# Kernel optimization log

Measured on AMD Instinct MI355X. Metric: run time of the kernel, lower is better.

The kernel has to match this reference:

```python
import jax, jax.numpy as jnp
import numpy as np

B, N, C = 2, 8192, 256
H = 8
CH = C // H  # head dim 32
M = 32       # nbhd size
HID = 512    # mlp hidden = 2.0 * dim
TAB = 3025   # pre_table rows (55x55 relative positions)
POSF = 5     # pos_dim + 3


def _ln(x, w, b):
    mu = jnp.mean(x, axis=-1, keepdims=True)
    var = jnp.var(x, axis=-1, keepdims=True)
    return (x - mu) / jnp.sqrt(var + 1e-5) * w + b


def setup_inputs() -> dict:
    key = jax.random.key(0)
    ks = jax.random.split(key, 24)
    s = lambda fan: 1.0 / np.sqrt(fan)
    inp = {
        'feat': jax.random.normal(ks[0], (B, N, C), jnp.float32),
        'member_idx': jax.random.randint(ks[1], (B, N, M), 0, N),
        'cluster_mask': jnp.ones((B, N, M), jnp.float32),
        'pe_idx': jax.random.randint(ks[2], (B, N, M), 0, TAB),
        'global_attn': 0,
        'pre_table': jax.random.normal(ks[3], (TAB, POSF), jnp.float32),
        'norm1_w': jnp.ones((C,), jnp.float32),
        'norm1_b': jnp.zeros((C,), jnp.float32),
        'q_w': jax.random.normal(ks[4], (C, C), jnp.float32) * s(C),
        'q_b': jnp.zeros((C,), jnp.float32),
        'kv_w': jax.random.normal(ks[5], (2 * C, C), jnp.float32) * s(C),
        'kv_b': jnp.zeros((2 * C,), jnp.float32),
        'blank_k': jax.random.normal(ks[6], (C,), jnp.float32),
        'blank_v': jax.random.normal(ks[7], (C,), jnp.float32),
        'pe_w': jax.random.normal(ks[8], (H, POSF), jnp.float32) * s(POSF),
        'pe_b': jnp.zeros((H,), jnp.float32),
        'proj_w': jax.random.normal(ks[9], (C, C), jnp.float32) * s(C),
        'proj_b': jnp.zeros((C,), jnp.float32),
        'norm2_w': jnp.ones((C,), jnp.float32),
        'norm2_b': jnp.zeros((C,), jnp.float32),
        'fc1_w': jax.random.normal(ks[10], (HID, C), jnp.float32) * s(C),
        'fc1_b': jnp.zeros((HID,), jnp.float32),
        'fc2_w': jax.random.normal(ks[11], (C, HID), jnp.float32) * s(HID),
        'fc2_b': jnp.zeros((C,), jnp.float32),
    }
    return inp


def _block(feat, member_idx, cluster_mask, pe_idx, pre_table,
           norm1_w, norm1_b, q_w, q_b, kv_w, kv_b, blank_k, blank_v,
           pe_w, pe_b, proj_w, proj_b, norm2_w, norm2_b,
           fc1_w, fc1_b, fc2_w, fc2_b):
    b, n, c = feat.shape
    h, c_ = H, c // H
    scale = c_ ** -0.5
    shortcut = feat
    x = _ln(feat, norm1_w, norm1_b)
    q = (x @ q_w.T + q_b) * scale                     # b n c
    kv = (x @ kv_w.T + kv_b).reshape(b, n, h, 2, c_)  # torch view layout
    k = kv[..., 0, :]                                 # b n h c_
    v = kv[..., 1, :]
    q = q.reshape(b, n, h, c_)
    bidx = jnp.arange(b)[:, None, None]
    k_g = k[bidx, member_idx]                         # b n m h c_ (gather)
    attn = jnp.einsum('bnhc,bnmhc->bhnm', q, k_g)     # CLUSTENQK
    pe_table = pre_table @ pe_w.T + pe_b              # TAB h
    pos = pe_table[pe_idx]                            # b n m h
    attn = attn + pos.transpose(0, 3, 1, 2)
    attn = attn + (1.0 - cluster_mask)[:, None, :, :] * (-100.0)
    blank = jnp.einsum('bnhc,hc->bhn', q, blank_k.reshape(h, c_))
    blank = jnp.clip(blank, -5.0, 5.0)[..., None]     # b h n 1
    attn = jnp.concatenate([attn, blank], axis=-1)
    attn = jax.nn.softmax(attn, axis=-1)
    blank_a = attn[..., -1:]
    attn = attn[..., :-1]
    v_g = v[bidx, member_idx]                         # b n m h c_
    out = jnp.einsum('bhnm,bnmhc->bnhc', attn, v_g)   # CLUSTENAV
    out = out + blank_a.transpose(0, 2, 1, 3) * blank_v.reshape(1, 1, h, c_)
    out = out.reshape(b, n, c)
    out = out @ proj_w.T + proj_b
    x = shortcut + out
    y = _ln(x, norm2_w, norm2_b)
    y = jax.nn.gelu(y @ fc1_w.T + fc1_b, approximate=False)
    y = y @ fc2_w.T + fc2_b
    return x + y


def reference(feat, member_idx, cluster_mask, pe_idx, global_attn, pre_table,
              norm1_w, norm1_b, q_w, q_b, kv_w, kv_b, blank_k, blank_v,
              pe_w, pe_b, proj_w, proj_b, norm2_w, norm2_b,
              fc1_w, fc1_b, fc2_w, fc2_b):
    # global_attn is False (local cluster attention path)
    return _block(feat, member_idx, cluster_mask, pe_idx, pre_table,
                  norm1_w, norm1_b, q_w, q_b, kv_w, kv_b, blank_k, blank_v,
                  pe_w, pe_b, proj_w, proj_b, norm2_w, norm2_b,
                  fc1_w, fc1_b, fc2_w, fc2_b)
```

## Files before the change

kernel.cpp:

```cpp
#include <hip/hip_runtime.h>
#include <math.h>

namespace {
constexpr int kN    = 8192;
constexpr int kC    = 256;
constexpr int kTAB  = 3025;
constexpr int kRowsTotal = 2 * kN;
constexpr float kScale = 0.17677669529663687f;
}

typedef __attribute__((ext_vector_type(8))) short bf16x8;
typedef __attribute__((ext_vector_type(4))) float f32x4;

__device__ __forceinline__ unsigned short f2bf(float f) {
  unsigned int u = __float_as_uint(f);
  u += 0x7fffu + ((u >> 16) & 1u);
  return (unsigned short)(u >> 16);
}
__device__ __forceinline__ float bflo(unsigned int u) {
  return __uint_as_float(u << 16);
}
__device__ __forceinline__ float bfhi(unsigned int u) {
  return __uint_as_float(u & 0xffff0000u);
}

#define GLOAD16(g, l)                                                   \
  __builtin_amdgcn_global_load_lds(                                     \
      (const __attribute__((address_space(1))) void*)(g),               \
      (__attribute__((address_space(3))) void*)(l), 16, 0, 0)

__global__ __launch_bounds__(256) void ln_bf16_kernel(
    const float* __restrict__ x, const float* __restrict__ w,
    const float* __restrict__ b, unsigned short* __restrict__ o) {
  int t = threadIdx.x;
  int row = blockIdx.x * 4 + (t >> 6);
  int l = t & 63;
  float4 v = *(const float4*)(x + (size_t)row * kC + l * 4);
  float s  = v.x + v.y + v.z + v.w;
  float s2 = v.x * v.x + v.y * v.y + v.z * v.z + v.w * v.w;
#pragma unroll
  for (int d = 1; d < 64; d <<= 1) {
    s  += __shfl_xor(s, d, 64);
    s2 += __shfl_xor(s2, d, 64);
  }
  float mu = s * (1.0f / kC);
  float rstd = rsqrtf(s2 * (1.0f / kC) - mu * mu + 1e-5f);
  float4 wv = *(const float4*)(w + l * 4);
  float4 bv = *(const float4*)(b + l * 4);
  unsigned short o0 = f2bf((v.x - mu) * rstd * wv.x + bv.x);
  unsigned short o1 = f2bf((v.y - mu) * rstd * wv.y + bv.y);
  unsigned short o2 = f2bf((v.z - mu) * rstd * wv.z + bv.z);
  unsigned short o3 = f2bf((v.w - mu) * rstd * wv.w + bv.w);
  uint2 ov;
  ov.x = ((unsigned int)o1 << 16) | o0;
  ov.y = ((unsigned int)o3 << 16) | o2;
  *(uint2*)(o + (size_t)row * kC + l * 4) = ov;
}

__global__ __launch_bounds__(256) void pe_kernel(const float* __restrict__ tab,
                                                 const float* __restrict__ pw,
                                                 const float* __restrict__ pb,
                                                 float* __restrict__ outp) {
  int i = blockIdx.x * 256 + threadIdx.x;
  if (i >= kTAB * 8) return;
  int r = i >> 3, h = i & 7;
  float acc = pb[h];
#pragma unroll
  for (int f = 0; f < 5; ++f) acc += tab[r * 5 + f] * pw[h * 5 + f];
  outp[i] = acc;
}

__global__ __launch_bounds__(256) void cast_weights_kernel(
    const float* __restrict__ qw, const float* __restrict__ kvw,
    const float* __restrict__ pjw, const float* __restrict__ f1w,
    const float* __restrict__ f2w, const float* __restrict__ qb,
    const float* __restrict__ kvb, unsigned short* __restrict__ wqkv,
    unsigned short* __restrict__ wproj, unsigned short* __restrict__ wfc1,
    unsigned short* __restrict__ wfc2, float* __restrict__ bqkv) {
  int i = blockIdx.x * 256 + threadIdx.x;
  if (i < 65536)       wqkv[i]            = f2bf(qw[i]);
  else if (i < 196608) wqkv[i]            = f2bf(kvw[i - 65536]);
  else if (i < 262144) wproj[i - 196608]  = f2bf(pjw[i - 196608]);
  else if (i < 393216) wfc1[i - 262144]   = f2bf(f1w[i - 262144]);
  else if (i < 524288) wfc2[i - 393216]   = f2bf(f2w[i - 393216]);
  else if (i < 524544) bqkv[i - 524288]   = qb[i - 524288];
  else if (i < 525056) bqkv[i - 524288]   = kvb[i - 524544];
}

template <int EPI, int KDIM>
__global__ __launch_bounds__(512) void gemm64(
    const unsigned short* __restrict__ A, const unsigned short* __restrict__ Wt,
    const float* __restrict__ bias, void* __restrict__ o1,
    unsigned short* __restrict__ o2, unsigned short* __restrict__ o3,
    const float* __restrict__ res, const float* __restrict__ w2,
    const float* __restrict__ b2, unsigned short* __restrict__ yln) {
  __shared__ alignas(16) unsigned short smem[40960];
  unsigned short* As0 = smem;
  unsigned short* Bs0 = smem + 8192;
  int t = threadIdx.x;
  int w = t >> 6, l = t & 63;
  int bm = blockIdx.x * 64, bn = blockIdx.y * 256;

  f32x4 acc[4][2] = {};

  const size_t aoff = (size_t)(bm + w * 8 + (l >> 3)) * KDIM + (l & 7) * 8;
  const size_t boff = (size_t)(bn + w * 32 + (l >> 3)) * KDIM + (l & 7) * 8;
  const int lr = l & 15, lk = l >> 4;

#define STAGE_T(buf, k0)                                                      \
  do {                                                                        \
    GLOAD16(A + aoff + (k0), As0 + (buf)*4096 + w * 512 + l * 8);             \
    GLOAD16(Wt + boff + (k0), Bs0 + (buf)*16384 + w * 2048 + l * 8);          \
    GLOAD16(Wt + boff + (k0) + (size_t)8 * KDIM,                              \
            Bs0 + (buf)*16384 + w * 2048 + 512 + l * 8);                      \
    GLOAD16(Wt + boff + (k0) + (size_t)16 * KDIM,                             \
            Bs0 + (buf)*16384 + w * 2048 + 1024 + l * 8);                     \
    GLOAD16(Wt + boff + (k0) + (size_t)24 * KDIM,                             \
            Bs0 + (buf)*16384 + w * 2048 + 1536 + l * 8);                     \
  } while (0)

  auto compute = [&](int buf) {
#pragma unroll
    for (int kk = 0; kk < 2; ++kk) {
      bf16x8 af[4], bfr[2];
#pragma unroll
      for (int mi = 0; mi < 4; ++mi)
        af[mi] = *(const bf16x8*)(As0 + buf * 4096 + (mi * 16 + lr) * 64 +
                                  kk * 32 + lk * 8);
#pragma unroll
      for (int ni = 0; ni < 2; ++ni)
        bfr[ni] = *(const bf16x8*)(Bs0 + buf * 16384 +
                                   (w * 32 + ni * 16 + lr) * 64 + kk * 32 +
                                   lk * 8);
#pragma unroll
      for (int mi = 0; mi < 4; ++mi)
#pragma unroll
        for (int ni = 0; ni < 2; ++ni)
          acc[mi][ni] = __builtin_amdgcn_mfma_f32_16x16x32_bf16(
              af[mi], bfr[ni], acc[mi][ni], 0, 0, 0);
    }
  };

  STAGE_T(0, 0);
  __syncthreads();
  int cur = 0;
#pragma unroll
  for (int k0 = 64; k0 < KDIM; k0 += 64) {
    STAGE_T(cur ^ 1, k0);
    compute(cur);
    __syncthreads();
    cur ^= 1;
  }
  compute(cur);

  if constexpr (EPI == 1) {
    __syncthreads();
    float* xs = (float*)smem;
#pragma unroll
    for (int mi = 0; mi < 4; ++mi) {
#pragma unroll
      for (int ni = 0; ni < 2; ++ni) {
        int c = w * 32 + ni * 16 + lr;
        float bv = bias[c];
#pragma unroll
        for (int j = 0; j < 4; ++j) {
          int rl = mi * 16 + lk * 4 + j;
          float x = acc[mi][ni][j] + bv + res[(size_t)(bm + rl) * 256 + c];
          xs[rl * 260 + c] = x;
          ((float*)o1)[(size_t)(bm + rl) * 256 + c] = x;
        }
      }
    }
    __syncthreads();
    int r = t >> 3, sub = t & 7;
    float4 xv[8];
    float sx = 0.f, sxx = 0.f;
#pragma unroll
    for (int i = 0; i < 8; ++i) {
      xv[i] = *(const float4*)&xs[r * 260 + sub * 4 + i * 32];
      sx  += xv[i].x + xv[i].y + xv[i].z + xv[i].w;
      sxx += xv[i].x * xv[i].x + xv[i].y * xv[i].y + xv[i].z * xv[i].z +
             xv[i].w * xv[i].w;
    }
#pragma unroll
    for (int d = 1; d < 8; d <<= 1) {
      sx  += __shfl_xor(sx, d, 64);
      sxx += __shfl_xor(sxx, d, 64);
    }
    float mu = sx * (1.0f / 256.0f);
    float rstd = rsqrtf(sxx * (1.0f / 256.0f) - mu * mu + 1e-5f);
#pragma unroll
    for (int i = 0; i < 8; ++i) {
      int c = sub * 4 + i * 32;
      float4 wv = *(const float4*)(w2 + c);
      float4 bv = *(const float4*)(b2 + c);
      unsigned short y0 = f2bf((xv[i].x - mu) * rstd * wv.x + bv.x);
      unsigned short y1 = f2bf((xv[i].y - mu) * rstd * wv.y + bv.y);
      unsigned short y2 = f2bf((xv[i].z - mu) * rstd * wv.z + bv.z);
      unsigned short y3 = f2bf((xv[i].w - mu) * rstd * wv.w + bv.w);
      uint2 ov;
      ov.x = ((unsigned int)y1 << 16) | y0;
      ov.y = ((unsigned int)y3 << 16) | y2;
      *(uint2*)(yln + (size_t)(bm + r) * 256 + c) = ov;
    }
  } else {
#pragma unroll
    for (int mi = 0; mi < 4; ++mi) {
#pragma unroll
      for (int ni = 0; ni < 2; ++ni) {
        int col = bn + w * 32 + ni * 16 + lr;
        float bv = bias[col];
#pragma unroll
        for (int j = 0; j < 4; ++j) {
          int rg = bm + mi * 16 + lk * 4 + j;
          float x = acc[mi][ni][j] + bv;
          if constexpr (EPI == 0) {
            if (col < 256) {
              ((unsigned short*)o1)[(size_t)rg * 256 + col] = f2bf(x * kScale);
            } else {
              int c = col - 256;
              int h = c >> 6, sbit = (c >> 5) & 1, ch = c & 31;
              unsigned short* dst = sbit ? o3 : o2;
              dst[(size_t)rg * 256 + h * 32 + ch] = f2bf(x);
            }
          } else if constexpr (EPI == 2) {
            float g = 0.5f * x * (1.0f + erff(x * 0.70710678118654752f));
            ((unsigned short*)o1)[(size_t)rg * 512 + col] = f2bf(g);
          } else {
            ((float*)o1)[(size_t)rg * 256 + col] =
                res[(size_t)rg * 256 + col] + x;
          }
        }
      }
    }
  }
#undef STAGE_T
}

__global__ __launch_bounds__(256) void attn_kernel(
    const unsigned short* __restrict__ q, const unsigned short* __restrict__ k,
    const unsigned short* __restrict__ v, const int* __restrict__ member_idx,
    const int* __restrict__ pe_idx, const float* __restrict__ cmask,
    const float* __restrict__ pe_full, const float* __restrict__ blank_k,
    const float* __restrict__ blank_v, unsigned short* __restrict__ outp) {
  int t = threadIdx.x;
  int w = t >> 6, l = t & 63;
  int bid = blockIdx.x;
  int part = bid & 7;
  int bb = part >> 2, hg = part & 3;
  int row = bb * kN + (bid >> 3) * 4 + w;
  const unsigned int kvbyte = (unsigned int)bb * (kN * 512u);
  const int hloc = l >> 5, m = l & 31;
  const int head = hg * 2 + hloc;

  __shared__ float        qs[4][64];
  __shared__ float        aw[4][2][34];
  __shared__ unsigned int offs[4][32];

  qs[w][l] = bflo((unsigned int)q[(size_t)row * 256 + hg * 64 + l]);
  int   idxv = member_idx[(size_t)row * 32 + m];
  float mk   = (1.0f - cmask[(size_t)row * 32 + m]) * -100.0f;
  float pe   = pe_full[(size_t)pe_idx[(size_t)row * 32 + m] * 8 + head];
  if (l < 32) offs[w][l] = kvbyte + (unsigned int)idxv * 512u;
  __syncthreads();

  float4 qv[8];
#pragma unroll
  for (int i = 0; i < 8; ++i) qv[i] = *(const float4*)&qs[w][hloc * 32 + i * 4];

  unsigned int koff = kvbyte + (unsigned int)idxv * 512u;
  const char* kp = (const char*)k + koff + head * 64;
  float lg = 0.f;
#pragma unroll
  for (int j = 0; j < 4; ++j) {
    uint4 u = *(const uint4*)(kp + j * 16);
    lg = fmaf(qv[2 * j].x, bflo(u.x), lg);
    lg = fmaf(qv[2 * j].y, bfhi(u.x), lg);
    lg = fmaf(qv[2 * j].z, bflo(u.y), lg);
    lg = fmaf(qv[2 * j].w, bfhi(u.y), lg);
    lg = fmaf(qv[2 * j + 1].x, bflo(u.z), lg);
    lg = fmaf(qv[2 * j + 1].y, bfhi(u.z), lg);
    lg = fmaf(qv[2 * j + 1].z, bflo(u.w), lg);
    lg = fmaf(qv[2 * j + 1].w, bfhi(u.w), lg);
  }
  lg += mk + pe;

  float bl = qs[w][hloc * 32 + m] * blank_k[head * 32 + m];
#pragma unroll
  for (int d = 1; d < 32; d <<= 1) bl += __shfl_xor(bl, d, 64);
  bl = fminf(fmaxf(bl, -5.0f), 5.0f);

  float mx = lg;
#pragma unroll
  for (int d = 1; d < 32; d <<= 1) mx = fmaxf(mx, __shfl_xor(mx, d, 64));
  mx = fmaxf(mx, bl);
  float e = __expf(lg - mx);
  float s = e;
#pragma unroll
  for (int d = 1; d < 32; d <<= 1) s += __shfl_xor(s, d, 64);
  float eb = __expf(bl - mx);
  s += eb;
  float inv = __builtin_amdgcn_rcpf(s);
  aw[w][hloc][m] = e * inv;
  if (m == 0) aw[w][hloc][32] = eb * inv;
  __syncthreads();

  const int hp = l >> 5, sq = (l >> 3) & 3, c8 = l & 7;
  const char* vb = (const char*)v + (hg * 2 + hp) * 64 + c8 * 8;
  float a0 = 0.f, a1 = 0.f, a2 = 0.f, a3 = 0.f;
#pragma unroll
  for (int i = 0; i < 8; ++i) {
    int mm = sq * 8 + i;
    float a = aw[w][hp][mm];
    uint2 u = *(const uint2*)(vb + offs[w][mm]);
    a0 = fmaf(a, bflo(u.x), a0);
    a1 = fmaf(a, bfhi(u.x), a1);
    a2 = fmaf(a, bflo(u.y), a2);
    a3 = fmaf(a, bfhi(u.y), a3);
  }
  a0 += __shfl_xor(a0, 8, 64);  a1 += __shfl_xor(a1, 8, 64);
  a2 += __shfl_xor(a2, 8, 64);  a3 += __shfl_xor(a3, 8, 64);
  a0 += __shfl_xor(a0, 16, 64); a1 += __shfl_xor(a1, 16, 64);
  a2 += __shfl_xor(a2, 16, 64); a3 += __shfl_xor(a3, 16, 64);
  if (sq == 0) {
    float ab = aw[w][hp][32];
    int c = (hg * 2 + hp) * 32 + c8 * 4;
    float4 bv = *(const float4*)(blank_v + c);
    a0 = fmaf(ab, bv.x, a0);
    a1 = fmaf(ab, bv.y, a1);
    a2 = fmaf(ab, bv.z, a2);
    a3 = fmaf(ab, bv.w, a3);
    uint2 o;
    o.x = ((unsigned int)f2bf(a1) << 16) | f2bf(a0);
    o.y = ((unsigned int)f2bf(a3) << 16) | f2bf(a2);
    *(uint2*)(outp + (size_t)row * 256 + c) = o;
  }
}

extern "C" void kernel_launch(void* const* d_in, const int* in_sizes, int n_in,
                              void* d_out, int out_size, void* d_ws, size_t ws_size,
                              hipStream_t stream) {
  const float* feat       = (const float*)d_in[0];
  const int*   member_idx = (const int*)d_in[1];
  const float* cmask      = (const float*)d_in[2];
  const int*   pe_idx     = (const int*)d_in[3];
  const float* pre_table  = (const float*)d_in[5];
  const float* n1w        = (const float*)d_in[6];
  const float* n1b        = (const float*)d_in[7];
  const float* q_w        = (const float*)d_in[8];
  const float* q_b        = (const float*)d_in[9];
  const float* kv_w       = (const float*)d_in[10];
  const float* kv_b       = (const float*)d_in[11];
  const float* blank_k    = (const float*)d_in[12];
  const float* blank_v    = (const float*)d_in[13];
  const float* pe_w       = (const float*)d_in[14];
  const float* pe_b       = (const float*)d_in[15];
  const float* proj_w     = (const float*)d_in[16];
  const float* proj_b     = (const float*)d_in[17];
  const float* n2w        = (const float*)d_in[18];
  const float* n2b        = (const float*)d_in[19];
  const float* fc1_w      = (const float*)d_in[20];
  const float* fc1_b      = (const float*)d_in[21];
  const float* fc2_w      = (const float*)d_in[22];
  const float* fc2_b      = (const float*)d_in[23];

  float* out = (float*)d_out;
  unsigned char* ws = (unsigned char*)d_ws;

  unsigned short* xln   = (unsigned short*)(ws + 0);
  unsigned short* q_buf = (unsigned short*)(ws + 8388608);
  unsigned short* k_buf = (unsigned short*)(ws + 16777216);
  unsigned short* v_buf = (unsigned short*)(ws + 25165824);
  unsigned short* wqkv  = (unsigned short*)(ws + 33554432);
  unsigned short* wproj = (unsigned short*)(ws + 33947648);
  unsigned short* wfc1  = (unsigned short*)(ws + 34078720);
  unsigned short* wfc2  = (unsigned short*)(ws + 34340864);
  float*          bqkv  = (float*)(ws + 34603008);
  float*          pe_buf= (float*)(ws + 34606080);
  unsigned short* attn_out = xln;
  unsigned short* yln   = q_buf;
  unsigned short* h1    = k_buf;

  cast_weights_kernel<<<2052, 256, 0, stream>>>(
      q_w, kv_w, proj_w, fc1_w, fc2_w, q_b, kv_b, wqkv, wproj, wfc1, wfc2, bqkv);
  pe_kernel<<<(kTAB * 8 + 255) / 256, 256, 0, stream>>>(pre_table, pe_w, pe_b, pe_buf);
  ln_bf16_kernel<<<kRowsTotal / 4, 256, 0, stream>>>(feat, n1w, n1b, xln);

  gemm64<0, 256><<<dim3(kRowsTotal / 64, 3), 512, 0, stream>>>(
      xln, wqkv, bqkv, q_buf, k_buf, v_buf, nullptr, nullptr, nullptr, nullptr);

  attn_kernel<<<kRowsTotal, 256, 0, stream>>>(
      q_buf, k_buf, v_buf, member_idx, pe_idx, cmask, pe_buf, blank_k, blank_v,
      attn_out);

  gemm64<1, 256><<<dim3(kRowsTotal / 64, 1), 512, 0, stream>>>(
      attn_out, wproj, proj_b, out, nullptr, nullptr, feat, n2w, n2b, yln);

  gemm64<2, 256><<<dim3(kRowsTotal / 64, 2), 512, 0, stream>>>(
      yln, wfc1, fc1_b, h1, nullptr, nullptr, nullptr, nullptr, nullptr, nullptr);

  gemm64<3, 512><<<dim3(kRowsTotal / 64, 1), 512, 0, stream>>>(
      h1, wfc2, fc2_b, out, nullptr, nullptr, out, nullptr, nullptr, nullptr);
}
```

Before: 131.1 us.

## Precompute per-row positional bias and restructure QK logit lanes for coalesced K loads

Adds a kernel that gathers the positional bias per (row, head, member) into a dense buffer, stored in the output array, before attention. This removes the double indirection through pe_idx inside the attention kernel. The QK logit computation is reorganised so each lane loads a 16-byte chunk across both heads of the group and reduces with a 4-lane shuffle, processing 4 members per lane. The goal is more coalesced K gathers and shorter reductions, at the cost of an extra launch and an extra 16 MB write/read of the positional buffer.

```diff
diff --git a/kernel.cpp b/kernel.cpp
--- a/kernel.cpp
+++ b/kernel.cpp
@@ -68,6 +68,15 @@
 #pragma unroll
   for (int f = 0; f < 5; ++f) acc += tab[r * 5 + f] * pw[h * 5 + f];
   outp[i] = acc;
+}
+
+__global__ __launch_bounds__(256) void pos_precompute_kernel(
+    const int* __restrict__ pe_idx, const float* __restrict__ pe_full,
+    float* __restrict__ pos_buf) {
+  int i = blockIdx.x * 256 + threadIdx.x;
+  int row = i >> 8, m = (i >> 3) & 31, h = i & 7;
+  int idx = pe_idx[(size_t)row * 32 + m];
+  pos_buf[(size_t)row * 256 + h * 32 + m] = pe_full[(size_t)idx * 8 + h];
 }
 
 __global__ __launch_bounds__(256) void cast_weights_kernel(
@@ -240,9 +249,9 @@
 __global__ __launch_bounds__(256) void attn_kernel(
     const unsigned short* __restrict__ q, const unsigned short* __restrict__ k,
     const unsigned short* __restrict__ v, const int* __restrict__ member_idx,
-    const int* __restrict__ pe_idx, const float* __restrict__ cmask,
-    const float* __restrict__ pe_full, const float* __restrict__ blank_k,
-    const float* __restrict__ blank_v, unsigned short* __restrict__ outp) {
+    const float* __restrict__ cmask, const float* __restrict__ pos_buf,
+    const float* __restrict__ blank_k, const float* __restrict__ blank_v,
+    unsigned short* __restrict__ outp) {
   int t = threadIdx.x;
   int w = t >> 6, l = t & 63;
   int bid = blockIdx.x;
@@ -250,59 +259,85 @@
   int bb = part >> 2, hg = part & 3;
   int row = bb * kN + (bid >> 3) * 4 + w;
   const unsigned int kvbyte = (unsigned int)bb * (kN * 512u);
-  const int hloc = l >> 5, m = l & 31;
-  const int head = hg * 2 + hloc;
 
   __shared__ float        qs[4][64];
-  __shared__ float        aw[4][2][34];
+  __shared__ float        aw[4][2][36];
   __shared__ unsigned int offs[4][32];
-
-  qs[w][l] = bflo((unsigned int)q[(size_t)row * 256 + hg * 64 + l]);
-  int   idxv = member_idx[(size_t)row * 32 + m];
-  float mk   = (1.0f - cmask[(size_t)row * 32 + m]) * -100.0f;
-  float pe   = pe_full[(size_t)pe_idx[(size_t)row * 32 + m] * 8 + head];
-  if (l < 32) offs[w][l] = kvbyte + (unsigned int)idxv * 512u;
+  __shared__ float        mkl[4][32];
+  __shared__ float        posl[4][2][32];
+
+  {
+    int m = l & 31, hloc = l >> 5;
+    qs[w][l] = bflo((unsigned int)q[(size_t)row * 256 + hg * 64 + l]);
+    posl[w][hloc][m] =
+        pos_buf[(size_t)row * 256 + (hg * 2 + hloc) * 32 + m];
+    if (l < 32) {
+      offs[w][l] = kvbyte + (unsigned int)member_idx[(size_t)row * 32 + l] * 512u;
+      mkl[w][l]  = (1.0f - cmask[(size_t)row * 32 + l]) * -100.0f;
+    }
+  }
   __syncthreads();
 
-  float4 qv[8];
-#pragma unroll
-  for (int i = 0; i < 8; ++i) qv[i] = *(const float4*)&qs[w][hloc * 32 + i * 4];
-
-  unsigned int koff = kvbyte + (unsigned int)idxv * 512u;
-  const char* kp = (const char*)k + koff + head * 64;
-  float lg = 0.f;
-#pragma unroll
-  for (int j = 0; j < 4; ++j) {
-    uint4 u = *(const uint4*)(kp + j * 16);
-    lg = fmaf(qv[2 * j].x, bflo(u.x), lg);
-    lg = fmaf(qv[2 * j].y, bfhi(u.x), lg);
-    lg = fmaf(qv[2 * j].z, bflo(u.y), lg);
-    lg = fmaf(qv[2 * j].w, bfhi(u.y), lg);
-    lg = fmaf(qv[2 * j + 1].x, bflo(u.z), lg);
-    lg = fmaf(qv[2 * j + 1].y, bfhi(u.z), lg);
-    lg = fmaf(qv[2 * j + 1].z, bflo(u.w), lg);
-    lg = fmaf(qv[2 * j + 1].w, bfhi(u.w), lg);
-  }
-  lg += mk + pe;
-
-  float bl = qs[w][hloc * 32 + m] * blank_k[head * 32 + m];
-#pragma unroll
-  for (int d = 1; d < 32; d <<= 1) bl += __shfl_xor(bl, d, 64);
-  bl = fminf(fmaxf(bl, -5.0f), 5.0f);
-
-  float mx = lg;
-#pragma unroll
-  for (int d = 1; d < 32; d <<= 1) mx = fmaxf(mx, __shfl_xor(mx, d, 64));
+  const int m8 = l >> 3, ch = l & 7;
+  const int hsel = ch >> 2;
+
+  float qv[8];
+  {
+    float4 a = *(const float4*)&qs[w][ch * 8];
+    float4 b = *(const float4*)&qs[w][ch * 8 + 4];
+    qv[0] = a.x; qv[1] = a.y; qv[2] = a.z; qv[3] = a.w;
+    qv[4] = b.x; qv[5] = b.y; qv[6] = b.z; qv[7] = b.w;
+  }
+
+  float lg[4];
+#pragma unroll
+  for (int i = 0; i < 4; ++i) {
+    int mi = i * 8 + m8;
+    const char* kp = (const char*)k + offs[w][mi] + hg * 128 + ch * 16;
+    uint4 u = *(const uint4*)kp;
+    float p = 0.f;
+    p = fmaf(qv[0], bflo(u.x), p);
+    p = fmaf(qv[1], bfhi(u.x), p);
+    p = fmaf(qv[2], bflo(u.y), p);
+    p = fmaf(qv[3], bfhi(u.y), p);
+    p = fmaf(qv[4], bflo(u.z), p);
+    p = fmaf(qv[5], bfhi(u.z), p);
+    p = fmaf(qv[6], bflo(u.w), p);
+    p = fmaf(qv[7], bfhi(u.w), p);
+    p += __shfl_xor(p, 1, 64);
+    p += __shfl_xor(p, 2, 64);
+    lg[i] = p + mkl[w][mi] + posl[w][hsel][mi];
+  }
+
+  float bl = 0.f;
+  {
+    const float* bk = blank_k + hg * 64 + ch * 8;
+#pragma unroll
+    for (int e = 0; e < 8; ++e) bl = fmaf(qv[e], bk[e], bl);
+    bl += __shfl_xor(bl, 1, 64);
+    bl += __shfl_xor(bl, 2, 64);
+    bl = fminf(fmaxf(bl, -5.0f), 5.0f);
+  }
+
+  float mx = fmaxf(fmaxf(lg[0], lg[1]), fmaxf(lg[2], lg[3]));
+  mx = fmaxf(mx, __shfl_xor(mx, 8, 64));
+  mx = fmaxf(mx, __shfl_xor(mx, 16, 64));
+  mx = fmaxf(mx, __shfl_xor(mx, 32, 64));
   mx = fmaxf(mx, bl);
-  float e = __expf(lg - mx);
-  float s = e;
-#pragma unroll
-  for (int d = 1; d < 32; d <<= 1) s += __shfl_xor(s, d, 64);
+  float e4[4], s = 0.f;
+#pragma unroll
+  for (int i = 0; i < 4; ++i) { e4[i] = __expf(lg[i] - mx); s += e4[i]; }
+  s += __shfl_xor(s, 8, 64);
+  s += __shfl_xor(s, 16, 64);
+  s += __shfl_xor(s, 32, 64);
   float eb = __expf(bl - mx);
   s += eb;
   float inv = __builtin_amdgcn_rcpf(s);
-  aw[w][hloc][m] = e * inv;
-  if (m == 0) aw[w][hloc][32] = eb * inv;
+  if ((ch & 3) == 0) {
+#pragma unroll
+    for (int i = 0; i < 4; ++i) aw[w][hsel][i * 8 + m8] = e4[i] * inv;
+    if (m8 == 0) aw[w][hsel][32] = eb * inv;
+  }
   __syncthreads();
 
   const int hp = l >> 5, sq = (l >> 3) & 3, c8 = l & 7;
@@ -380,17 +415,19 @@
   unsigned short* attn_out = xln;
   unsigned short* yln   = q_buf;
   unsigned short* h1    = k_buf;
+  float*          pos_buf = out;
 
   cast_weights_kernel<<<2052, 256, 0, stream>>>(
       q_w, kv_w, proj_w, fc1_w, fc2_w, q_b, kv_b, wqkv, wproj, wfc1, wfc2, bqkv);
   pe_kernel<<<(kTAB * 8 + 255) / 256, 256, 0, stream>>>(pre_table, pe_w, pe_b, pe_buf);
   ln_bf16_kernel<<<kRowsTotal / 4, 256, 0, stream>>>(feat, n1w, n1b, xln);
+  pos_precompute_kernel<<<kRowsTotal, 256, 0, stream>>>(pe_idx, pe_buf, pos_buf);
 
   gemm64<0, 256><<<dim3(kRowsTotal / 64, 3), 512, 0, stream>>>(
       xln, wqkv, bqkv, q_buf, k_buf, v_buf, nullptr, nullptr, nullptr, nullptr);
 
   attn_kernel<<<kRowsTotal, 256, 0, stream>>>(
-      q_buf, k_buf, v_buf, member_idx, pe_idx, cmask, pe_buf, blank_k, blank_v,
+      q_buf, k_buf, v_buf, member_idx, cmask, pos_buf, blank_k, blank_v,
       attn_out);
 
   gemm64<1, 256><<<dim3(kRowsTotal / 64, 1), 512, 0, stream>>>(
```

Result: no change. 130.4 us (-0.5%).
